# Optimization experiments

Measured on AMD Instinct MI355X. Metric: run time of the kernel, lower is better.

Reference implementation:

```python
import jax, jax.numpy as jnp
import numpy as np

D_MODEL = 512
NUM_HEADS = 8
HEAD_DIM = D_MODEL // NUM_HEADS
CTX = 20
EPS = 1e-5


def _layernorm(x, w, b):
    mu = jnp.mean(x, axis=-1, keepdims=True)
    var = jnp.var(x, axis=-1, keepdims=True)
    return (x - mu) * jax.lax.rsqrt(var + EPS) * w + b


def setup_inputs() -> dict:
    key = jax.random.key(0)
    ks = jax.random.split(key, 12)
    B, T = 4096, CTX
    s_attn = 1.0 / np.sqrt(D_MODEL)
    s_ffn1 = 1.0 / np.sqrt(D_MODEL)
    s_ffn2 = 1.0 / np.sqrt(4 * D_MODEL)
    return {
        "x": jax.random.normal(ks[0], (B, T, D_MODEL), dtype=jnp.float32),
        "ln1_w": jnp.ones((D_MODEL,), jnp.float32),
        "ln1_b": jnp.zeros((D_MODEL,), jnp.float32),
        # per-head projections stacked: [H, D, head_dim]
        "Wq": jax.random.normal(ks[1], (NUM_HEADS, D_MODEL, HEAD_DIM), dtype=jnp.float32) * s_attn,
        "Wk": jax.random.normal(ks[2], (NUM_HEADS, D_MODEL, HEAD_DIM), dtype=jnp.float32) * s_attn,
        "Wv": jax.random.normal(ks[3], (NUM_HEADS, D_MODEL, HEAD_DIM), dtype=jnp.float32) * s_attn,
        "Wo": jax.random.normal(ks[4], (D_MODEL, D_MODEL), dtype=jnp.float32) * s_attn,
        "Wo_b": jnp.zeros((D_MODEL,), jnp.float32),
        "ln2_w": jnp.ones((D_MODEL,), jnp.float32),
        "ln2_b": jnp.zeros((D_MODEL,), jnp.float32),
        "W1": jax.random.normal(ks[5], (D_MODEL, 4 * D_MODEL), dtype=jnp.float32) * s_ffn1,
        "b1": jnp.zeros((4 * D_MODEL,), jnp.float32),
        "W2": jax.random.normal(ks[6], (4 * D_MODEL, D_MODEL), dtype=jnp.float32) * s_ffn2,
        "b2": jnp.zeros((D_MODEL,), jnp.float32),
    }


def reference(x, ln1_w, ln1_b, Wq, Wk, Wv, Wo, Wo_b, ln2_w, ln2_b, W1, b1, W2, b2):
    B, T, D = x.shape
    # --- multi-head attention (dropout = identity, eval mode) ---
    h = _layernorm(x, ln1_w, ln1_b)
    # [B,T,D] x [H,D,hd] -> [B,H,T,hd]
    q = jnp.einsum('btd,hde->bhte', h, Wq)
    k = jnp.einsum('btd,hde->bhte', h, Wk)
    v = jnp.einsum('btd,hde->bhte', h, Wv)
    scores = jnp.einsum('bhte,bhse->bhts', q, k) / np.sqrt(HEAD_DIM)
    mask = jnp.tril(jnp.ones((T, T), dtype=bool))
    scores = jnp.where(mask, scores, -jnp.inf)
    attn = jax.nn.softmax(scores, axis=-1)
    ctx = jnp.einsum('bhts,bhse->bhte', attn, v)  # [B,H,T,hd]
    # concat heads along last dim (head order matches torch cat)
    ctx = jnp.transpose(ctx, (0, 2, 1, 3)).reshape(B, T, D)
    attn_out = ctx @ Wo.T + Wo_b
    x = x + attn_out
    # --- FFN ---
    h2 = _layernorm(x, ln2_w, ln2_b)
    ff = jax.nn.relu(h2 @ W1 + b1) @ W2 + b2
    return x + ff
```

## Files before the change

kernel.cpp:

```cpp
#include <hip/hip_runtime.h>

typedef __attribute__((ext_vector_type(8))) short short8;
typedef __attribute__((ext_vector_type(4))) float float4v;

__device__ __forceinline__ float b2f(ushort u) {
  union { uint i; float f; } c; c.i = ((uint)u) << 16; return c.f;
}
__device__ __forceinline__ ushort f2b(float f) {
  union { float f; uint i; } c; c.f = f;
  return (ushort)((c.i + 0x7fffu + ((c.i >> 16) & 1u)) >> 16);
}
__device__ __forceinline__ float ldin(const void* p, size_t i, int f32) {
  return f32 ? ((const float*)p)[i] : b2f(((const ushort*)p)[i]);
}
__device__ __forceinline__ void load_lds16(const ushort* g, ushort* l) {
  __builtin_amdgcn_global_load_lds((__attribute__((address_space(1))) const void*)g,
                                   (__attribute__((address_space(3))) void*)l, 16, 0, 0);
}
typedef __attribute__((address_space(3))) const ushort* lds_cp;
__device__ __forceinline__ short8 ldsr128(const ushort* p) {
  short8 r;
  asm volatile("ds_read_b128 %0, %1" : "=v"(r) : "v"((lds_cp)p));
  return r;
}
__device__ __forceinline__ void wg_barrier() {
  asm volatile("" ::: "memory");
  __builtin_amdgcn_s_barrier();
  asm volatile("" ::: "memory");
}

__global__ void detect(const void* w1, int* flag) {
  const uint u = *(const uint*)w1;
  *flag = (u == 0x3F800000u) ? 1 : 0;
}

__global__ __launch_bounds__(512, 2) void gemm256(
    const ushort* __restrict__ A, const ushort* __restrict__ B,
    void* C, const ushort* __restrict__ bias, const void* res,
    const int* resflagp, const int* outflagp,
    int M, int N, int K, int relu, int nb)
{
  __shared__ ushort lA[2][256 * 64];
  __shared__ ushort lB[2][256 * 64];
  const int tid = threadIdx.x;
  const int w = tid >> 6, l = tid & 63;
  const int wr = w >> 2, wc = w & 3;
  const int bid = blockIdx.x;
  const int low3 = bid & 7, rest = bid >> 3;
  const int n_idx = rest % nb;
  const int band  = ((rest / nb) << 3) | low3;
  const int mBase = band * 256;
  const int nBase = n_idx * 256;
  const int lrow = l >> 3;
  const int lcolsw = (((l & 7) ^ lrow) * 8);
  const int cs0 = (((l >> 4) + 0) ^ (l & 7)) << 3;
  const int cs1 = (((l >> 4) + 4) ^ (l & 7)) << 3;
  const int arow0 = wr * 128 + (l & 15);
  const int brow0 = wc * 64 + (l & 15);
  const int NT = K >> 6;

  auto STAGE = [&](const ushort* __restrict__ Gp, int rb, ushort* ldsOp, int segBase, int kof) {
#pragma unroll
    for (int j = 0; j < 2; ++j) {
      const int s = segBase + j * 8 + w;
      load_lds16(Gp + (size_t)(rb + s * 8 + lrow) * K + kof + lcolsw, ldsOp + s * 512);
    }
  };

  const float4v vz = {0.f, 0.f, 0.f, 0.f};
  float4v acc[8][4];
#pragma unroll
  for (int i = 0; i < 8; ++i)
#pragma unroll
    for (int j = 0; j < 4; ++j) acc[i][j] = vz;

  STAGE(A, mBase, &lA[0][0], 0, 0);  STAGE(A, mBase, &lA[0][0], 16, 0);
  STAGE(B, nBase, &lB[0][0], 0, 0);  STAGE(B, nBase, &lB[0][0], 16, 0);
  const int kp1 = (NT > 1 ? 64 : 0);
  STAGE(B, nBase, &lB[1][0], 0, kp1); STAGE(B, nBase, &lB[1][0], 16, kp1);

  short8 bf[4][2], af[2][2];

  for (int t = 0; t < NT; ++t) {
    const int cur = t & 1;
    ushort* lAc = &lA[cur][0];
    ushort* lAn = &lA[cur ^ 1][0];
    ushort* lBc = &lB[cur][0];
    const int kA1 = (t + 1 < NT ? t + 1 : NT - 1) << 6;
    const int kB2 = (t + 2 < NT ? t + 2 : NT - 1) << 6;

    STAGE(A, mBase, lAn, 0, kA1);
    asm volatile("s_waitcnt vmcnt(6)" ::: "memory");
    __builtin_amdgcn_sched_barrier(0);
    wg_barrier();
#pragma unroll
    for (int nj = 0; nj < 4; ++nj) {
      bf[nj][0] = ldsr128(&lBc[(brow0 + nj * 16) * 64 + cs0]);
      bf[nj][1] = ldsr128(&lBc[(brow0 + nj * 16) * 64 + cs1]);
    }
    af[0][0] = ldsr128(&lAc[(arow0 + 0) * 64 + cs0]);
    af[0][1] = ldsr128(&lAc[(arow0 + 0) * 64 + cs1]);
    af[1][0] = ldsr128(&lAc[(arow0 + 16) * 64 + cs0]);
    af[1][1] = ldsr128(&lAc[(arow0 + 16) * 64 + cs1]);
    asm volatile("s_waitcnt lgkmcnt(0)" ::: "memory");
    __builtin_amdgcn_sched_barrier(0);
    __builtin_amdgcn_s_setprio(1);
#pragma unroll
    for (int i = 0; i < 2; ++i)
#pragma unroll
      for (int nj = 0; nj < 4; ++nj) {
        acc[i][nj] = __builtin_amdgcn_mfma_f32_16x16x32_bf16(af[i][0], bf[nj][0], acc[i][nj], 0, 0, 0);
        acc[i][nj] = __builtin_amdgcn_mfma_f32_16x16x32_bf16(af[i][1], bf[nj][1], acc[i][nj], 0, 0, 0);
      }
    __builtin_amdgcn_s_setprio(0);
    wg_barrier();

#pragma unroll
    for (int p = 1; p < 4; ++p) {
      if (p == 1)      STAGE(A, mBase, lAn, 16, kA1);
      else if (p == 2) STAGE(B, nBase, lBc, 0, kB2);
      else             STAGE(B, nBase, lBc, 16, kB2);
      af[0][0] = ldsr128(&lAc[(arow0 + (2 * p) * 16) * 64 + cs0]);
      af[0][1] = ldsr128(&lAc[(arow0 + (2 * p) * 16) * 64 + cs1]);
      af[1][0] = ldsr128(&lAc[(arow0 + (2 * p + 1) * 16) * 64 + cs0]);
      af[1][1] = ldsr128(&lAc[(arow0 + (2 * p + 1) * 16) * 64 + cs1]);
      wg_barrier();
      asm volatile("s_waitcnt lgkmcnt(0)" ::: "memory");
      __builtin_amdgcn_sched_barrier(0);
      __builtin_amdgcn_s_setprio(1);
#pragma unroll
      for (int i = 0; i < 2; ++i)
#pragma unroll
        for (int nj = 0; nj < 4; ++nj) {
          acc[2 * p + i][nj] = __builtin_amdgcn_mfma_f32_16x16x32_bf16(af[i][0], bf[nj][0], acc[2 * p + i][nj], 0, 0, 0);
          acc[2 * p + i][nj] = __builtin_amdgcn_mfma_f32_16x16x32_bf16(af[i][1], bf[nj][1], acc[2 * p + i][nj], 0, 0, 0);
        }
      __builtin_amdgcn_s_setprio(0);
      wg_barrier();
    }
  }
  asm volatile("s_waitcnt vmcnt(0)" ::: "memory");
  __builtin_amdgcn_sched_barrier(0);

  const int rf32 = (res && resflagp) ? *resflagp : 0;
  const int of32 = outflagp ? *outflagp : 0;
  const int r0 = mBase + wr * 128 + (l >> 4) * 4;
  const int c0 = nBase + wc * 64 + (l & 15);
#pragma unroll
  for (int nj = 0; nj < 4; ++nj) {
    const int col = c0 + nj * 16;
    const float bv = bias ? b2f(bias[col]) : 0.f;
#pragma unroll
    for (int mi = 0; mi < 8; ++mi) {
#pragma unroll
      for (int rr = 0; rr < 4; ++rr) {
        const size_t off = (size_t)(r0 + mi * 16 + rr) * N + col;
        float v = acc[mi][nj][rr] + bv;
        if (res) v += rf32 ? ((const float*)res)[off] : b2f(((const ushort*)res)[off]);
        if (relu) v = fmaxf(v, 0.f);
        if (of32) ((float*)C)[off] = v;
        else      ((ushort*)C)[off] = f2b(v);
      }
    }
  }
}

__global__ __launch_bounds__(256) void lnorm(const void* __restrict__ x,
                                             const ushort* __restrict__ gw,
                                             const ushort* __restrict__ gb,
                                             ushort* __restrict__ out,
                                             ushort* __restrict__ xcopy,
                                             const int* flagp)
{
  const int f32 = flagp ? *flagp : 0;
  const int tok = blockIdx.x * 4 + (threadIdx.x >> 6);
  const int l = threadIdx.x & 63;
  const size_t base = (size_t)tok * 512 + l * 8;
  float v[8];
  if (f32) {
    const float4* p = (const float4*)((const float*)x + base);
    float4 a = p[0], b = p[1];
    v[0]=a.x; v[1]=a.y; v[2]=a.z; v[3]=a.w; v[4]=b.x; v[5]=b.y; v[6]=b.z; v[7]=b.w;
  } else {
    uint4 u = *(const uint4*)((const ushort*)x + base);
    uint uu[4] = {u.x, u.y, u.z, u.w};
#pragma unroll
    for (int i = 0; i < 4; ++i) {
      v[2*i]   = b2f((ushort)(uu[i] & 0xffffu));
      v[2*i+1] = b2f((ushort)(uu[i] >> 16));
    }
  }
  if (xcopy) {
    uint xo[4];
#pragma unroll
    for (int i = 0; i < 4; ++i)
      xo[i] = (uint)f2b(v[2*i]) | ((uint)f2b(v[2*i+1]) << 16);
    uint4 xv; xv.x = xo[0]; xv.y = xo[1]; xv.z = xo[2]; xv.w = xo[3];
    *(uint4*)(xcopy + base) = xv;
  }
  float s = 0.f, ss = 0.f;
#pragma unroll
  for (int i = 0; i < 8; ++i) { s += v[i]; ss += v[i] * v[i]; }
  for (int off = 32; off > 0; off >>= 1) {
    s  += __shfl_xor(s, off, 64);
    ss += __shfl_xor(ss, off, 64);
  }
  const float mean = s * (1.f / 512.f);
  const float var  = ss * (1.f / 512.f) - mean * mean;
  const float inv  = rsqrtf(var + 1e-5f);
  uint4 uwv = *(const uint4*)(gw + l * 8);
  uint4 ubv = *(const uint4*)(gb + l * 8);
  uint uws[4] = {uwv.x, uwv.y, uwv.z, uwv.w};
  uint ubs[4] = {ubv.x, ubv.y, ubv.z, ubv.w};
  uint ro[4];
#pragma unroll
  for (int i = 0; i < 4; ++i) {
    float w0 = b2f((ushort)(uws[i] & 0xffffu)), w1 = b2f((ushort)(uws[i] >> 16));
    float b0 = b2f((ushort)(ubs[i] & 0xffffu)), b1 = b2f((ushort)(ubs[i] >> 16));
    float y0 = (v[2*i]   - mean) * inv * w0 + b0;
    float y1 = (v[2*i+1] - mean) * inv * w1 + b1;
    ro[i] = (uint)f2b(y0) | ((uint)f2b(y1) << 16);
  }
  uint4 o; o.x = ro[0]; o.y = ro[1]; o.z = ro[2]; o.w = ro[3];
  *(uint4*)(out + base) = o;
}

__global__ __launch_bounds__(128) void attn(const ushort* __restrict__ QKV,
                                            ushort* __restrict__ ctx)
{
  __shared__ float sq[2][20][65];
  __shared__ float sk[2][20][65];
  __shared__ float sv[2][20][65];
  __shared__ float sp[2][20][33];
  const int w = threadIdx.x >> 6;
  const int l = threadIdx.x & 63;
  const int idx = blockIdx.x * 2 + w;
  const int b = idx >> 3, h = idx & 7;
  const ushort* base = QKV + (size_t)b * 20 * 1536 + h * 64;
#pragma unroll
  for (int tp = 0; tp < 10; ++tp) {
    const int t = tp * 2 + (l >> 5);
    const int e2 = (l & 31) * 2;
    const uint uq = *(const uint*)&base[t * 1536 + e2];
    const uint uk = *(const uint*)&base[t * 1536 + 512 + e2];
    const uint uv = *(const uint*)&base[t * 1536 + 1024 + e2];
    sq[w][t][e2] = b2f((ushort)(uq & 0xffffu)); sq[w][t][e2+1] = b2f((ushort)(uq >> 16));
    sk[w][t][e2] = b2f((ushort)(uk & 0xffffu)); sk[w][t][e2+1] = b2f((ushort)(uk >> 16));
    sv[w][t][e2] = b2f((ushort)(uv & 0xffffu)); sv[w][t][e2+1] = b2f((ushort)(uv >> 16));
  }
  __syncthreads();
  for (int tp = 0; tp < 10; ++tp) {
    const int t = tp * 2 + (l >> 5);
    const int s = l & 31;
    const int sr = (s < 20) ? s : 19;
    float d = 0.f;
#pragma unroll 8
    for (int e = 0; e < 64; ++e) d += sq[w][t][e] * sk[w][sr][e];
    const bool valid = (s <= t) && (s < 20);
    float sc = valid ? d * 0.125f : -1e30f;
    float m = sc;
    for (int off = 16; off > 0; off >>= 1) m = fmaxf(m, __shfl_xor(m, off, 32));
    float p = valid ? __expf(sc - m) : 0.f;
    float sum = p;
    for (int off = 16; off > 0; off >>= 1) sum += __shfl_xor(sum, off, 32);
    if (s < 20) sp[w][t][s] = p / sum;
  }
  __syncthreads();
  ushort* cbase = ctx + (size_t)b * 20 * 512 + h * 64 + l;
  for (int t = 0; t < 20; ++t) {
    float o = 0.f;
    for (int s = 0; s <= t; ++s) o += sp[w][t][s] * sv[w][s][l];
    cbase[t * 512] = f2b(o);
  }
}

__global__ __launch_bounds__(256) void pack_w(
    const void* Wq, const void* Wk, const void* Wv, const void* Wo,
    const void* W1, const void* W2,
    const void* ln1w, const void* ln1b, const void* ln2w, const void* ln2b,
    const void* Wob, const void* b1v, const void* b2v,
    const int* flagp,
    ushort* __restrict__ Wqkv_t, ushort* __restrict__ W1_t,
    ushort* __restrict__ W2_t, ushort* __restrict__ Wo_c,
    ushort* __restrict__ smalls)
{
  const int f32 = *flagp;
  const int i = blockIdx.x * 256 + threadIdx.x;
  if (i < 786432) {
    const int m = i / 262144;
    const int r = i - m * 262144;
    const void* src = (m == 0) ? Wq : ((m == 1) ? Wk : Wv);
    const int hh = r >> 15, d = (r >> 6) & 511, e = r & 63;
    Wqkv_t[(size_t)(m * 512 + hh * 64 + e) * 512 + d] = f2b(ldin(src, r, f32));
  } else if (i < 1835008) {
    const int r = i - 786432;
    const int d = r >> 11, f = r & 2047;
    W1_t[(size_t)f * 512 + d] = f2b(ldin(W1, r, f32));
  } else if (i < 2883584) {
    const int r = i - 1835008;
    const int f = r >> 9, o = r & 511;
    W2_t[(size_t)o * 2048 + f] = f2b(ldin(W2, r, f32));
  } else if (i < 3145728) {
    const int r = i - 2883584;
    Wo_c[r] = f2b(ldin(Wo, r, f32));
  } else {
    const int r = i - 3145728;
    const void* src; int idx;
    if      (r < 512)  { src = ln1w; idx = r; }
    else if (r < 1024) { src = ln1b; idx = r - 512; }
    else if (r < 1536) { src = ln2w; idx = r - 1024; }
    else if (r < 2048) { src = ln2b; idx = r - 1536; }
    else if (r < 2560) { src = Wob;  idx = r - 2048; }
    else if (r < 3072) { src = b2v;  idx = r - 2560; }
    else               { src = b1v;  idx = r - 3072; }
    smalls[r] = f2b(ldin(src, idx, f32));
  }
}

extern "C" void kernel_launch(void* const* d_in, const int* in_sizes, int n_in,
                              void* d_out, int out_size, void* d_ws, size_t ws_size,
                              hipStream_t stream) {
  char* ws = (char*)d_ws;
  int*    flag   = (int*)ws;
  ushort* Wqkv_t = (ushort*)(ws + 4096);
  ushort* W1_t   = (ushort*)(ws + 1576960ull);
  ushort* W2_t   = (ushort*)(ws + 3674112ull);
  ushort* Wo_c   = (ushort*)(ws + 5771264ull);
  ushort* smalls = (ushort*)(ws + 6295552ull);
  ushort* QKV    = (ushort*)(ws + 8388608ull);
  ushort* ff1    = QKV;
  ushort* ctxb   = (ushort*)(ws + 260046848ull);
  ushort* h      = (ushort*)(ws + 343932928ull);
  ushort* x2     = (ushort*)(ws + 427819008ull);
  ushort* xbf    = (ushort*)(ws + 511705088ull);
  const bool have_xbf = ws_size >= 595591168ull;

  detect<<<1, 1, 0, stream>>>(d_in[1], flag);
  pack_w<<<12308, 256, 0, stream>>>(d_in[3], d_in[4], d_in[5], d_in[6],
                                    d_in[10], d_in[12],
                                    d_in[1], d_in[2], d_in[8], d_in[9],
                                    d_in[7], d_in[11], d_in[13],
                                    flag, Wqkv_t, W1_t, W2_t, Wo_c, smalls);
  lnorm<<<20480, 256, 0, stream>>>(d_in[0], smalls + 0, smalls + 512, h,
                                   have_xbf ? xbf : nullptr, flag);
  gemm256<<<6 * 320, 512, 0, stream>>>(h, Wqkv_t, QKV, nullptr, nullptr,
                                       nullptr, nullptr, 81920, 1536, 512, 0, 6);
  attn<<<16384, 128, 0, stream>>>(QKV, ctxb);
  gemm256<<<2 * 320, 512, 0, stream>>>(ctxb, Wo_c, x2, smalls + 2048,
                                       have_xbf ? (const void*)xbf : (const void*)d_in[0],
                                       have_xbf ? nullptr : flag, nullptr,
                                       81920, 512, 512, 0, 2);
  lnorm<<<20480, 256, 0, stream>>>(x2, smalls + 1024, smalls + 1536, h, nullptr, nullptr);
  gemm256<<<8 * 320, 512, 0, stream>>>(h, W1_t, ff1, smalls + 3072, nullptr,
                                       nullptr, nullptr, 81920, 2048, 512, 1, 8);
  gemm256<<<2 * 320, 512, 0, stream>>>(ff1, W2_t, d_out, smalls + 2560, x2,
                                       nullptr, flag, 81920, 512, 2048, 0, 2);
}
```

Baseline: 1.735 ms.

## Software-pipeline LDS fragment reads ahead of MFMA blocks in gemm256

Restructures the GEMM main loop so the A fragments for the next MFMA sub-block are read from LDS into a second register set while the current sub-block computes. The B fragments and first A fragments for the next K-tile are prefetched at the end of each iteration. This hides LDS read latency behind MFMA work, at the cost of extra registers for the doubled A fragments and changed vmcnt/barrier placement.

```diff
diff --git a/kernel.cpp b/kernel.cpp
--- a/kernel.cpp
+++ b/kernel.cpp
@@ -33,6 +33,31 @@
   const uint u = *(const uint*)w1;
   *flag = (u == 0x3F800000u) ? 1 : 0;
 }
+
+#define RDA(DST, LP, RB)                                            \
+  DST[0][0] = ldsr128(&(LP)[(arow0 + (RB)) * 64 + cs0]);            \
+  DST[0][1] = ldsr128(&(LP)[(arow0 + (RB)) * 64 + cs1]);            \
+  DST[1][0] = ldsr128(&(LP)[(arow0 + (RB) + 16) * 64 + cs0]);       \
+  DST[1][1] = ldsr128(&(LP)[(arow0 + (RB) + 16) * 64 + cs1]);
+#define RDB(LP)                                                     \
+  _Pragma("unroll")                                                 \
+  for (int nj = 0; nj < 4; ++nj) {                                  \
+    bf[nj][0] = ldsr128(&(LP)[(brow0 + nj * 16) * 64 + cs0]);       \
+    bf[nj][1] = ldsr128(&(LP)[(brow0 + nj * 16) * 64 + cs1]);       \
+  }
+#define MM8(MI, AF)                                                 \
+  _Pragma("unroll")                                                 \
+  for (int i = 0; i < 2; ++i)                                       \
+    _Pragma("unroll")                                               \
+    for (int nj = 0; nj < 4; ++nj) {                                \
+      acc[(MI) + i][nj] = __builtin_amdgcn_mfma_f32_16x16x32_bf16(  \
+          AF[i][0], bf[nj][0], acc[(MI) + i][nj], 0, 0, 0);         \
+      acc[(MI) + i][nj] = __builtin_amdgcn_mfma_f32_16x16x32_bf16(  \
+          AF[i][1], bf[nj][1], acc[(MI) + i][nj], 0, 0, 0);         \
+    }
+#define WAIT_LGKM0()                                  \
+  asm volatile("s_waitcnt lgkmcnt(0)" ::: "memory");  \
+  __builtin_amdgcn_sched_barrier(0);
 
 __global__ __launch_bounds__(512, 2) void gemm256(
     const ushort* __restrict__ A, const ushort* __restrict__ B,
@@ -78,65 +103,62 @@
   STAGE(B, nBase, &lB[0][0], 0, 0);  STAGE(B, nBase, &lB[0][0], 16, 0);
   const int kp1 = (NT > 1 ? 64 : 0);
   STAGE(B, nBase, &lB[1][0], 0, kp1); STAGE(B, nBase, &lB[1][0], 16, kp1);
-
-  short8 bf[4][2], af[2][2];
+  asm volatile("s_waitcnt vmcnt(4)" ::: "memory");
+  __builtin_amdgcn_sched_barrier(0);
+  wg_barrier();
+
+  short8 bf[4][2], af0[2][2], af1[2][2];
+  RDB((&lB[0][0]));
+  RDA(af0, (&lA[0][0]), 0);
 
   for (int t = 0; t < NT; ++t) {
     const int cur = t & 1;
     ushort* lAc = &lA[cur][0];
     ushort* lAn = &lA[cur ^ 1][0];
     ushort* lBc = &lB[cur][0];
+    ushort* lBn = &lB[cur ^ 1][0];
     const int kA1 = (t + 1 < NT ? t + 1 : NT - 1) << 6;
     const int kB2 = (t + 2 < NT ? t + 2 : NT - 1) << 6;
 
     STAGE(A, mBase, lAn, 0, kA1);
-    asm volatile("s_waitcnt vmcnt(6)" ::: "memory");
+    wg_barrier();
+    WAIT_LGKM0();
+    __builtin_amdgcn_s_setprio(1);
+    MM8(0, af0);
+    __builtin_amdgcn_s_setprio(0);
+    RDA(af1, lAc, 32);
+    wg_barrier();
+
+    STAGE(A, mBase, lAn, 16, kA1);
+    wg_barrier();
+    WAIT_LGKM0();
+    __builtin_amdgcn_s_setprio(1);
+    MM8(2, af1);
+    __builtin_amdgcn_s_setprio(0);
+    RDA(af0, lAc, 64);
+    wg_barrier();
+
+    STAGE(B, nBase, lBc, 0, kB2);
+    wg_barrier();
+    WAIT_LGKM0();
+    __builtin_amdgcn_s_setprio(1);
+    MM8(4, af0);
+    __builtin_amdgcn_s_setprio(0);
+    RDA(af1, lAc, 96);
+    wg_barrier();
+
+    STAGE(B, nBase, lBc, 16, kB2);
+    wg_barrier();
+    WAIT_LGKM0();
+    __builtin_amdgcn_s_setprio(1);
+    MM8(6, af1);
+    __builtin_amdgcn_s_setprio(0);
+    asm volatile("s_waitcnt vmcnt(4)" ::: "memory");
     __builtin_amdgcn_sched_barrier(0);
     wg_barrier();
-#pragma unroll
-    for (int nj = 0; nj < 4; ++nj) {
-      bf[nj][0] = ldsr128(&lBc[(brow0 + nj * 16) * 64 + cs0]);
-      bf[nj][1] = ldsr128(&lBc[(brow0 + nj * 16) * 64 + cs1]);
-    }
-    af[0][0] = ldsr128(&lAc[(arow0 + 0) * 64 + cs0]);
-    af[0][1] = ldsr128(&lAc[(arow0 + 0) * 64 + cs1]);
-    af[1][0] = ldsr128(&lAc[(arow0 + 16) * 64 + cs0]);
-    af[1][1] = ldsr128(&lAc[(arow0 + 16) * 64 + cs1]);
-    asm volatile("s_waitcnt lgkmcnt(0)" ::: "memory");
-    __builtin_amdgcn_sched_barrier(0);
-    __builtin_amdgcn_s_setprio(1);
-#pragma unroll
-    for (int i = 0; i < 2; ++i)
-#pragma unroll
-      for (int nj = 0; nj < 4; ++nj) {
-        acc[i][nj] = __builtin_amdgcn_mfma_f32_16x16x32_bf16(af[i][0], bf[nj][0], acc[i][nj], 0, 0, 0);
-        acc[i][nj] = __builtin_amdgcn_mfma_f32_16x16x32_bf16(af[i][1], bf[nj][1], acc[i][nj], 0, 0, 0);
-      }
-    __builtin_amdgcn_s_setprio(0);
-    wg_barrier();
-
-#pragma unroll
-    for (int p = 1; p < 4; ++p) {
-      if (p == 1)      STAGE(A, mBase, lAn, 16, kA1);
-      else if (p == 2) STAGE(B, nBase, lBc, 0, kB2);
-      else             STAGE(B, nBase, lBc, 16, kB2);
-      af[0][0] = ldsr128(&lAc[(arow0 + (2 * p) * 16) * 64 + cs0]);
-      af[0][1] = ldsr128(&lAc[(arow0 + (2 * p) * 16) * 64 + cs1]);
-      af[1][0] = ldsr128(&lAc[(arow0 + (2 * p + 1) * 16) * 64 + cs0]);
-      af[1][1] = ldsr128(&lAc[(arow0 + (2 * p + 1) * 16) * 64 + cs1]);
-      wg_barrier();
-      asm volatile("s_waitcnt lgkmcnt(0)" ::: "memory");
-      __builtin_amdgcn_sched_barrier(0);
-      __builtin_amdgcn_s_setprio(1);
-#pragma unroll
-      for (int i = 0; i < 2; ++i)
-#pragma unroll
-        for (int nj = 0; nj < 4; ++nj) {
-          acc[2 * p + i][nj] = __builtin_amdgcn_mfma_f32_16x16x32_bf16(af[i][0], bf[nj][0], acc[2 * p + i][nj], 0, 0, 0);
-          acc[2 * p + i][nj] = __builtin_amdgcn_mfma_f32_16x16x32_bf16(af[i][1], bf[nj][1], acc[2 * p + i][nj], 0, 0, 0);
-        }
-      __builtin_amdgcn_s_setprio(0);
-      wg_barrier();
+    if (t + 1 < NT) {
+      RDB(lBn);
+      RDA(af0, lAn, 0);
     }
   }
   asm volatile("s_waitcnt vmcnt(0)" ::: "memory");
```

Measured after the change: 1.733 ms. Within noise of the previous version (-0.1%).
